# Kernel tuning notes

Measured on AMD Instinct MI355X. Metric: run time of the kernel, lower is better.

The kernel has to match this reference:

```python
import jax, jax.numpy as jnp
import numpy as np

B, S, D, H, HID = 4, 1024, 1024, 16, 4096
DK = D // H
EPS = 1e-6


def _ln(x):
    # LayerNorm without affine, eps=1e-6
    mu = jnp.mean(x, axis=-1, keepdims=True)
    var = jnp.var(x, axis=-1, keepdims=True)
    return (x - mu) / jnp.sqrt(var + EPS)


def _lin(x, W, b):
    # torch Linear convention: W is [out, in]
    y = jnp.einsum('...i,oi->...o', x, W)
    return y + b if b is not None else y


def setup_inputs() -> dict:
    key = jax.random.key(0)
    ks = jax.random.split(key, 16)
    sc = lambda fan_in: 1.0 / np.sqrt(fan_in)
    inp = {
        'x': jax.random.normal(ks[0], (B, S, D), jnp.float32),
        'cond': jax.random.normal(ks[1], (B, 1, D), jnp.float32),
        'Wq': jax.random.normal(ks[2], (D, D), jnp.float32) * sc(D),
        'bq': jnp.zeros((D,), jnp.float32),
        'Wk': jax.random.normal(ks[3], (D, D), jnp.float32) * sc(D),
        'bk': jnp.zeros((D,), jnp.float32),
        'Wv': jax.random.normal(ks[4], (D, D), jnp.float32) * sc(D),
        'bv': jnp.zeros((D,), jnp.float32),
        'Wo': jax.random.normal(ks[5], (D, D), jnp.float32) * sc(D),
        'bo': jnp.zeros((D,), jnp.float32),
        'W1': jax.random.normal(ks[6], (HID, D), jnp.float32) * sc(D),
        'b1': jnp.zeros((HID,), jnp.float32),
        'W2': jax.random.normal(ks[7], (D, HID), jnp.float32) * sc(HID),
        'b2': jnp.zeros((D,), jnp.float32),
        'Wada': jax.random.normal(ks[8], (6 * D, D), jnp.float32) * sc(D),
        'bada': jnp.zeros((6 * D,), jnp.float32),
    }
    return inp


def reference(x, cond, Wq, bq, Wk, bk, Wv, bv, Wo, bo, W1, b1, W2, b2, Wada, bada):
    # adaLN modulation: SiLU -> Linear -> chunk 6 along last dim
    mod = _lin(jax.nn.silu(cond), Wada, bada)  # [B,1,6D]
    gama1, beta1, alpha1, gama2, beta2, alpha2 = jnp.split(mod, 6, axis=-1)

    # attention branch
    residual = x
    h = _ln(x) * (1.0 + beta1) + gama1  # modulate(shift=gama1, scale=beta1)
    q = _lin(h, Wq, bq).reshape(B, S, H, DK)
    k = _lin(h, Wk, bk).reshape(B, S, H, DK)
    v = _lin(h, Wv, bv).reshape(B, S, H, DK)
    scores = jnp.einsum('bqhd,bkhd->bhqk', q, k) / jnp.sqrt(jnp.float32(DK))
    probs = jax.nn.softmax(scores, axis=-1)
    attn = jnp.einsum('bhqk,bkhd->bqhd', probs, v).reshape(B, S, D)
    attn = _lin(attn, Wo, bo)
    x = residual + alpha1 * attn

    # MLP branch
    residual = x
    h = _ln(x) * (1.0 + beta2) + gama2
    h = _lin(h, W1, b1)
    h = jax.nn.gelu(h, approximate=False)  # torch nn.GELU default (erf)
    h = _lin(h, W2, b2)
    return residual + alpha2 * h
```

## Files before the change

### kernel.cpp

```cpp
#include <hip/hip_runtime.h>
#include <cstdint>

typedef __bf16 bf16_t;
typedef __bf16 bf16x4 __attribute__((ext_vector_type(4)));
typedef __bf16 bf16x8 __attribute__((ext_vector_type(8)));
typedef float f32x4 __attribute__((ext_vector_type(4)));

#define B_ 4
#define S_ 1024
#define D_ 1024
#define HID_ 4096
#define MEG (1u << 20)

static const size_t OFF_WBF  = 0;
static const size_t OFF_BQKV = 25165824;
static const size_t OFF_MOD  = 25178112;
static const size_t OFF_H    = 25276416;
static const size_t OFF_QKV  = 33665024;
static const size_t OFF_VT   = 58830848;
static const size_t OFF_ATTN = 67219456;
static const size_t OFF_X1   = 75608064;
static const size_t OFF_PART = 92385280;
static const size_t OFF_MLPH = 159494144;

__device__ __forceinline__ void async_copy16(const bf16_t* g, bf16_t* l) {
  __builtin_amdgcn_global_load_lds(
      (__attribute__((address_space(1))) void*)(g),
      (__attribute__((address_space(3))) void*)(l), 16, 0, 0);
}

__global__ __launch_bounds__(256) void convert_pack(
    const float* __restrict__ Wq, const float* __restrict__ Wk,
    const float* __restrict__ Wv, const float* __restrict__ Wo,
    const float* __restrict__ W1, const float* __restrict__ W2,
    const float* __restrict__ bq, const float* __restrict__ bk,
    const float* __restrict__ bv, bf16_t* __restrict__ wbf,
    float* __restrict__ bqkv) {
  const int y = blockIdx.y;
  if (y == 6) {
    int i = blockIdx.x * 256 + threadIdx.x;
    if (i < 3072)
      bqkv[i] = i < 1024 ? bq[i] : (i < 2048 ? bk[i - 1024] : bv[i - 2048]);
    return;
  }
  const float* src; bf16_t* dst; int n;
  switch (y) {
    case 0: src = Wq; dst = wbf;           n = MEG;     break;
    case 1: src = Wk; dst = wbf + MEG;     n = MEG;     break;
    case 2: src = Wv; dst = wbf + 2*MEG;   n = MEG;     break;
    case 3: src = Wo; dst = wbf + 3*MEG;   n = MEG;     break;
    case 4: src = W1; dst = wbf + 4*MEG;   n = 4*MEG;   break;
    default: src = W2; dst = wbf + 8*MEG;  n = 4*MEG;   break;
  }
  int idx = (blockIdx.x * 256 + threadIdx.x) * 4;
  if (idx < n) {
    float4 v = *(const float4*)(src + idx);
    bf16x4 pk;
    pk.x = (__bf16)v.x; pk.y = (__bf16)v.y; pk.z = (__bf16)v.z; pk.w = (__bf16)v.w;
    *(bf16x4*)(dst + idx) = pk;
  }
}

__global__ __launch_bounds__(256) void ada_mod(
    const float* __restrict__ cond, const float* __restrict__ Wada,
    const float* __restrict__ bada, float* __restrict__ mod) {
  const int wave = threadIdx.x >> 6, lane = threadIdx.x & 63;
  const int gw = blockIdx.x * 4 + wave;
  const int b = gw / 6144, o = gw % 6144;
  const float* cb = cond + b * D_;
  const float* wr = Wada + (size_t)o * D_;
  float acc = 0.f;
#pragma unroll
  for (int l = 0; l < 16; l++) {
    int i = l * 64 + lane;
    float c = cb[i];
    float s = c / (1.0f + __expf(-c));
    acc += s * wr[i];
  }
#pragma unroll
  for (int offs = 32; offs; offs >>= 1) acc += __shfl_xor(acc, offs);
  if (lane == 0) mod[gw] = acc + bada[o];
}

__global__ __launch_bounds__(256) void ln_modulate(
    const float* __restrict__ X, const float* __restrict__ mod,
    bf16_t* __restrict__ H, int goff) {
  const int row = blockIdx.x;
  const int b = row >> 10;
  const int t = threadIdx.x;
  const float* xr = X + (size_t)row * D_;
  float4 xv = *(const float4*)(xr + t * 4);
  float s = xv.x + xv.y + xv.z + xv.w;
  float q = xv.x*xv.x + xv.y*xv.y + xv.z*xv.z + xv.w*xv.w;
  const int wave = t >> 6, lane = t & 63;
#pragma unroll
  for (int offs = 32; offs; offs >>= 1) {
    s += __shfl_down(s, offs);
    q += __shfl_down(q, offs);
  }
  __shared__ float sb[4][2];
  if (lane == 0) { sb[wave][0] = s; sb[wave][1] = q; }
  __syncthreads();
  float st = sb[0][0] + sb[1][0] + sb[2][0] + sb[3][0];
  float qt = sb[0][1] + sb[1][1] + sb[2][1] + sb[3][1];
  float mu = st * (1.0f / D_);
  float var = qt * (1.0f / D_) - mu * mu;
  float rstd = rsqrtf(var + 1e-6f);
  const float* mb = mod + (size_t)b * 6144 + goff;
  const int c = t * 4;
  float4 gm = *(const float4*)(mb + c);
  float4 bt = *(const float4*)(mb + 1024 + c);
  bf16x4 pk;
  pk.x = (__bf16)((xv.x - mu) * rstd * (1.0f + bt.x) + gm.x);
  pk.y = (__bf16)((xv.y - mu) * rstd * (1.0f + bt.y) + gm.y);
  pk.z = (__bf16)((xv.z - mu) * rstd * (1.0f + bt.z) + gm.z);
  pk.w = (__bf16)((xv.w - mu) * rstd * (1.0f + bt.w) + gm.w);
  *(bf16x4*)(H + (size_t)row * D_ + c) = pk;
}

__global__ __launch_bounds__(256) void transpose_v(
    const bf16_t* __restrict__ qkv, bf16_t* __restrict__ vT) {
  __shared__ bf16_t tile[64][65];
  const int bh = blockIdx.y;
  const int b = bh >> 4, hh = bh & 15;
  const int s0 = blockIdx.x * 64;
  const int t = threadIdx.x;
  const int tx = t & 63, ty = t >> 6;
  const bf16_t* src = qkv + (size_t)b * S_ * 3072 + 2048 + hh * 64;
  for (int r = ty; r < 64; r += 4)
    tile[r][tx] = src[(size_t)(s0 + r) * 3072 + tx];
  __syncthreads();
  bf16_t* dst = vT + (size_t)bh * 64 * 1024;
  for (int r = ty; r < 64; r += 4)
    dst[(size_t)r * 1024 + s0 + tx] = tile[tx][r];
}

__global__ __launch_bounds__(256) void flash_attn(
    const bf16_t* __restrict__ qkv, const bf16_t* __restrict__ vT,
    bf16_t* __restrict__ attn) {
  __shared__ __align__(16) bf16_t Qs[64 * 64];
  __shared__ __align__(16) bf16_t Ks[128 * 64];
  __shared__ __align__(16) bf16_t Vs[64 * 128];
  __shared__ __align__(16) bf16_t Ps[4 * 16 * 136];

  const int t = threadIdx.x;
  const int wave = t >> 6, lane = t & 63;
  const int lm = lane & 15, quad = lane >> 4;
  const int bh = blockIdx.y;
  const int b = bh >> 4, hh = bh & 15;
  const int s0 = blockIdx.x * 64;

  const bf16_t* qbase = qkv + (size_t)b * S_ * 3072 + hh * 64;
  const bf16_t* kbase = qbase + 1024;
  const bf16_t* vbase = vT + (size_t)bh * (64 * 1024);

#pragma unroll
  for (int j = 0; j < 2; j++) {
    int slot = j * 256 + t;
    int row = slot >> 3;
    int cg = (slot & 7) ^ (row & 7);
    async_copy16(qbase + (size_t)(s0 + row) * 3072 + cg * 8, &Qs[slot * 8]);
  }

  f32x4 accO[4] = {};
  float mrow[4], lrow[4];
#pragma unroll
  for (int r = 0; r < 4; r++) { mrow[r] = -1e30f; lrow[r] = 0.f; }

  bf16_t* Pw = &Ps[wave * 16 * 136];

  for (int k0 = 0; k0 < S_; k0 += 128) {
    __syncthreads();
#pragma unroll
    for (int j = 0; j < 4; j++) {
      int slot = j * 256 + t;
      int row = slot >> 3;
      int cg = (slot & 7) ^ (row & 7);
      async_copy16(kbase + (size_t)(k0 + row) * 3072 + cg * 8, &Ks[slot * 8]);
    }
#pragma unroll
    for (int j = 0; j < 4; j++) {
      int slot = j * 256 + t;
      int row = slot >> 4;
      int cp = slot & 15;
      int cg = (cp & 8) | ((cp & 7) ^ (row & 7));
      async_copy16(vbase + (size_t)row * 1024 + k0 + cg * 8, &Vs[slot * 8]);
    }
    __syncthreads();

    f32x4 accS[8] = {};
#pragma unroll
    for (int ks = 0; ks < 2; ks++) {
      int rq = wave * 16 + lm;
      int cq = (ks * 4 + quad) ^ (rq & 7);
      bf16x8 aq = *(const bf16x8*)&Qs[rq * 64 + cq * 8];
#pragma unroll
      for (int ni = 0; ni < 8; ni++) {
        int rk = ni * 16 + lm;
        int ck = (ks * 4 + quad) ^ (rk & 7);
        bf16x8 bk8 = *(const bf16x8*)&Ks[rk * 64 + ck * 8];
        accS[ni] = __builtin_amdgcn_mfma_f32_16x16x32_bf16(aq, bk8, accS[ni], 0, 0, 0);
      }
    }

    float alpha[4];
#pragma unroll
    for (int r = 0; r < 4; r++) {
      float mx = accS[0][r];
#pragma unroll
      for (int ni = 1; ni < 8; ni++) mx = fmaxf(mx, accS[ni][r]);
      mx = fmaxf(mx, __shfl_xor(mx, 1));
      mx = fmaxf(mx, __shfl_xor(mx, 2));
      mx = fmaxf(mx, __shfl_xor(mx, 4));
      mx = fmaxf(mx, __shfl_xor(mx, 8));
      mx *= 0.125f;
      float mnew = fmaxf(mrow[r], mx);
      alpha[r] = __expf(mrow[r] - mnew);
      mrow[r] = mnew;
      float sum = 0.f;
#pragma unroll
      for (int ni = 0; ni < 8; ni++) {
        float p = __expf(accS[ni][r] * 0.125f - mnew);
        accS[ni][r] = p;
        sum += p;
      }
      sum += __shfl_xor(sum, 1);
      sum += __shfl_xor(sum, 2);
      sum += __shfl_xor(sum, 4);
      sum += __shfl_xor(sum, 8);
      lrow[r] = lrow[r] * alpha[r] + sum;
    }
#pragma unroll
    for (int di = 0; di < 4; di++)
#pragma unroll
      for (int r = 0; r < 4; r++) accO[di][r] *= alpha[r];

#pragma unroll
    for (int ni = 0; ni < 8; ni++)
#pragma unroll
      for (int r = 0; r < 4; r++)
        Pw[(quad * 4 + r) * 136 + ni * 16 + lm] = (__bf16)accS[ni][r];

#pragma unroll
    for (int ks2 = 0; ks2 < 4; ks2++) {
      bf16x8 ap = *(const bf16x8*)&Pw[lm * 136 + ks2 * 32 + quad * 8];
#pragma unroll
      for (int di = 0; di < 4; di++) {
        int rv = di * 16 + lm;
        int g = ks2 * 4 + quad;
        int cp = (g & 8) | ((g & 7) ^ (rv & 7));
        bf16x8 bv = *(const bf16x8*)&Vs[rv * 128 + cp * 8];
        accO[di] = __builtin_amdgcn_mfma_f32_16x16x32_bf16(ap, bv, accO[di], 0, 0, 0);
      }
    }
  }

#pragma unroll
  for (int r = 0; r < 4; r++) {
    float inv = 1.0f / lrow[r];
    int row = quad * 4 + r;
#pragma unroll
    for (int di = 0; di < 4; di++) {
      int col = di * 16 + lm;
      int cph = (col >> 3) ^ (row & 7);
      Pw[row * 64 + cph * 8 + (col & 7)] = (__bf16)(accO[di][r] * inv);
    }
  }
  bf16_t* abase = attn + (size_t)b * S_ * 1024 +
                  (size_t)(s0 + wave * 16) * 1024 + hh * 64;
#pragma unroll
  for (int it = 0; it < 2; it++) {
    int slot = it * 64 + lane;
    int row = slot >> 3;
    int cg = slot & 7;
    int cph = cg ^ (row & 7);
    bf16x8 val = *(const bf16x8*)&Pw[row * 64 + cph * 8];
    *(bf16x8*)(abase + (size_t)row * 1024 + cg * 8) = val;
  }
}

template <int EPI>
__global__ __launch_bounds__(256) void gemm_bt(
    const bf16_t* __restrict__ A, int lda, long long sAz,
    const bf16_t* __restrict__ B, int ldb, long long sBz,
    void* __restrict__ Cv, int ldc, long long sCz,
    int M, int N, int K,
    const float* __restrict__ bias,
    float scale) {
  __shared__ __align__(16) bf16_t As[2][128 * 32];
  __shared__ __align__(16) bf16_t Bs[2][128 * 32];

  const int z = blockIdx.z;
  A += (size_t)z * sAz;
  B += (size_t)z * sBz;

  const int t = threadIdx.x;
  const int wave = t >> 6;
  const int lane = t & 63;
  const int lm = lane & 15;
  const int quad = lane >> 4;
  const int wr = wave >> 1;
  const int wc = wave & 1;

  const int m0 = blockIdx.y * 128;
  const int n0 = blockIdx.x * 128;

  f32x4 acc[4][4] = {};

  const int srow = t >> 2;
  const int gch = (t & 3) ^ (srow & 3);
  const int lds_off = t * 8;
  const bf16_t* Ap0 = A + (size_t)(m0 + srow) * lda + gch * 8;
  const bf16_t* Ap1 = A + (size_t)(m0 + 64 + srow) * lda + gch * 8;
  const bf16_t* Bp0 = B + (size_t)(n0 + srow) * ldb + gch * 8;
  const bf16_t* Bp1 = B + (size_t)(n0 + 64 + srow) * ldb + gch * 8;

  const int niter = K >> 5;
  async_copy16(Ap0, &As[0][lds_off]);
  async_copy16(Ap1, &As[0][2048 + lds_off]);
  async_copy16(Bp0, &Bs[0][lds_off]);
  async_copy16(Bp1, &Bs[0][2048 + lds_off]);

  for (int it = 0; it < niter; ++it) {
    asm volatile("s_waitcnt vmcnt(0)\n\ts_barrier" ::: "memory");
    if (it + 1 < niter) {
      const int ko = (it + 1) << 5;
      const int nb = (it + 1) & 1;
      async_copy16(Ap0 + ko, &As[nb][lds_off]);
      async_copy16(Ap1 + ko, &As[nb][2048 + lds_off]);
      async_copy16(Bp0 + ko, &Bs[nb][lds_off]);
      async_copy16(Bp1 + ko, &Bs[nb][2048 + lds_off]);
    }
    const int cb = it & 1;
    bf16x8 af[4], bfr[4];
#pragma unroll
    for (int i = 0; i < 4; i++) {
      int ra = wr * 64 + i * 16 + lm;
      af[i] = *(const bf16x8*)&As[cb][ra * 32 + ((quad ^ (ra & 3)) * 8)];
      int rb = wc * 64 + i * 16 + lm;
      bfr[i] = *(const bf16x8*)&Bs[cb][rb * 32 + ((quad ^ (rb & 3)) * 8)];
    }
#pragma unroll
    for (int mi = 0; mi < 4; mi++)
#pragma unroll
      for (int ni = 0; ni < 4; ni++)
        acc[mi][ni] = __builtin_amdgcn_mfma_f32_16x16x32_bf16(
            af[mi], bfr[ni], acc[mi][ni], 0, 0, 0);
  }

  const size_t cz = (size_t)z * sCz;
#pragma unroll
  for (int mi = 0; mi < 4; mi++) {
#pragma unroll
    for (int ni = 0; ni < 4; ni++) {
#pragma unroll
      for (int r = 0; r < 4; r++) {
        int row = m0 + wr * 64 + mi * 16 + quad * 4 + r;
        int col = n0 + wc * 64 + ni * 16 + lm;
        float v = acc[mi][ni][r];
        size_t idx = cz + (size_t)row * ldc + col;
        if (EPI == 1) {
          ((float*)Cv)[idx] = v * scale;
        } else if (EPI == 0) {
          if (bias) v += bias[col];
          ((bf16_t*)Cv)[idx] = (__bf16)v;
        } else if (EPI == 3) {
          v += bias[col];
          float u = 1.5957691216f * (v + 0.044715f * v * v * v);
          float g = v / (1.0f + __expf(-u));
          ((bf16_t*)Cv)[idx] = (__bf16)g;
        }
      }
    }
  }
}

__global__ __launch_bounds__(256) void reduce_ln(
    const float* __restrict__ part, const float* __restrict__ x,
    const float* __restrict__ bo, const float* __restrict__ mod,
    float* __restrict__ x1, bf16_t* __restrict__ h) {
  const int row = blockIdx.x;
  const int b = row >> 10;
  const int t = threadIdx.x;
  const int c = t * 4;
  const size_t idx = (size_t)row * 1024 + c;
  float4 p0 = *(const float4*)(part + idx);
  float4 p1 = *(const float4*)(part + 4194304 + idx);
  float4 bb = *(const float4*)(bo + c);
  float4 al = *(const float4*)(mod + (size_t)b * 6144 + 2048 + c);
  float4 xs = *(const float4*)(x + idx);
  float4 xv;
  xv.x = xs.x + al.x * (p0.x + p1.x + bb.x);
  xv.y = xs.y + al.y * (p0.y + p1.y + bb.y);
  xv.z = xs.z + al.z * (p0.z + p1.z + bb.z);
  xv.w = xs.w + al.w * (p0.w + p1.w + bb.w);
  *(float4*)(x1 + idx) = xv;

  float s = xv.x + xv.y + xv.z + xv.w;
  float q = xv.x*xv.x + xv.y*xv.y + xv.z*xv.z + xv.w*xv.w;
  const int wave = t >> 6, lane = t & 63;
#pragma unroll
  for (int offs = 32; offs; offs >>= 1) {
    s += __shfl_down(s, offs);
    q += __shfl_down(q, offs);
  }
  __shared__ float sb[4][2];
  if (lane == 0) { sb[wave][0] = s; sb[wave][1] = q; }
  __syncthreads();
  float st = sb[0][0] + sb[1][0] + sb[2][0] + sb[3][0];
  float qt = sb[0][1] + sb[1][1] + sb[2][1] + sb[3][1];
  float mu = st * (1.0f / D_);
  float var = qt * (1.0f / D_) - mu * mu;
  float rstd = rsqrtf(var + 1e-6f);
  const float* mb = mod + (size_t)b * 6144 + 3072;
  float4 gm = *(const float4*)(mb + c);
  float4 bt = *(const float4*)(mb + 1024 + c);
  bf16x4 pk;
  pk.x = (__bf16)((xv.x - mu) * rstd * (1.0f + bt.x) + gm.x);
  pk.y = (__bf16)((xv.y - mu) * rstd * (1.0f + bt.y) + gm.y);
  pk.z = (__bf16)((xv.z - mu) * rstd * (1.0f + bt.z) + gm.z);
  pk.w = (__bf16)((xv.w - mu) * rstd * (1.0f + bt.w) + gm.w);
  *(bf16x4*)(h + idx) = pk;
}

__global__ __launch_bounds__(256) void reduce_w2(
    const float* __restrict__ part, const float* __restrict__ x1,
    const float* __restrict__ b2, const float* __restrict__ mod,
    float* __restrict__ out) {
  const int idx = (blockIdx.x * 256 + threadIdx.x) * 4;
  const int col = idx & 1023;
  const int row = idx >> 10;
  const int b = row >> 10;
  float4 s0 = *(const float4*)(part + idx);
  float4 s1 = *(const float4*)(part + 4194304 + idx);
  float4 s2 = *(const float4*)(part + 8388608 + idx);
  float4 s3 = *(const float4*)(part + 12582912 + idx);
  float4 bb = *(const float4*)(b2 + col);
  float4 al = *(const float4*)(mod + (size_t)b * 6144 + 5120 + col);
  float4 rs = *(const float4*)(x1 + idx);
  float4 o;
  o.x = rs.x + al.x * (s0.x + s1.x + s2.x + s3.x + bb.x);
  o.y = rs.y + al.y * (s0.y + s1.y + s2.y + s3.y + bb.y);
  o.z = rs.z + al.z * (s0.z + s1.z + s2.z + s3.z + bb.z);
  o.w = rs.w + al.w * (s0.w + s1.w + s2.w + s3.w + bb.w);
  *(float4*)(out + idx) = o;
}

extern "C" void kernel_launch(void* const* d_in, const int* in_sizes, int n_in,
                              void* d_out, int out_size, void* d_ws, size_t ws_size,
                              hipStream_t stream) {
  (void)in_sizes; (void)n_in; (void)out_size; (void)ws_size;
  const float* x    = (const float*)d_in[0];
  const float* cond = (const float*)d_in[1];
  const float* Wq   = (const float*)d_in[2];
  const float* bq   = (const float*)d_in[3];
  const float* Wk   = (const float*)d_in[4];
  const float* bk   = (const float*)d_in[5];
  const float* Wv   = (const float*)d_in[6];
  const float* bv   = (const float*)d_in[7];
  const float* Wo   = (const float*)d_in[8];
  const float* bo   = (const float*)d_in[9];
  const float* W1   = (const float*)d_in[10];
  const float* b1   = (const float*)d_in[11];
  const float* W2   = (const float*)d_in[12];
  const float* b2   = (const float*)d_in[13];
  const float* Wada = (const float*)d_in[14];
  const float* bada = (const float*)d_in[15];

  uint8_t* ws = (uint8_t*)d_ws;
  bf16_t* wbf   = (bf16_t*)(ws + OFF_WBF);
  float*  bqkv  = (float*)(ws + OFF_BQKV);
  float*  mod   = (float*)(ws + OFF_MOD);
  bf16_t* h     = (bf16_t*)(ws + OFF_H);
  bf16_t* qkv   = (bf16_t*)(ws + OFF_QKV);
  bf16_t* vT    = (bf16_t*)(ws + OFF_VT);
  bf16_t* attn  = (bf16_t*)(ws + OFF_ATTN);
  float*  x1    = (float*)(ws + OFF_X1);
  float*  part  = (float*)(ws + OFF_PART);
  bf16_t* mlph  = (bf16_t*)(ws + OFF_MLPH);
  float* out = (float*)d_out;

  convert_pack<<<dim3(4096, 7, 1), 256, 0, stream>>>(Wq, Wk, Wv, Wo, W1, W2,
                                                     bq, bk, bv, wbf, bqkv);
  ada_mod<<<6144, 256, 0, stream>>>(cond, Wada, bada, mod);
  ln_modulate<<<4096, 256, 0, stream>>>(x, mod, h, 0);
  gemm_bt<0><<<dim3(24, 32, 1), 256, 0, stream>>>(
      h, 1024, 0, wbf, 1024, 0, qkv, 3072, 0, 4096, 3072, 1024,
      bqkv, 1.f);
  transpose_v<<<dim3(16, 64, 1), 256, 0, stream>>>(qkv, vT);
  flash_attn<<<dim3(16, 64, 1), 256, 0, stream>>>(qkv, vT, attn);

  gemm_bt<1><<<dim3(8, 32, 2), 256, 0, stream>>>(
      attn, 1024, 512, wbf + (size_t)3 * MEG, 1024, 512, part, 1024, 4194304,
      4096, 1024, 512, nullptr, 1.f);
  reduce_ln<<<4096, 256, 0, stream>>>(part, x, bo, mod, x1, h);

  gemm_bt<3><<<dim3(32, 32, 1), 256, 0, stream>>>(
      h, 1024, 0, wbf + (size_t)4 * MEG, 1024, 0, mlph, 4096, 0,
      4096, 4096, 1024, b1, 1.f);
  gemm_bt<1><<<dim3(8, 32, 4), 256, 0, stream>>>(
      mlph, 4096, 1024, wbf + (size_t)8 * MEG, 4096, 1024, part, 1024, 4194304,
      4096, 1024, 1024, nullptr, 1.f);
  reduce_w2<<<4096, 256, 0, stream>>>(part, x1, b2, mod, out);
}
```

Baseline: 429.1 us.

## Remap GEMM tiles per XCD, retune LDS swizzle, halve W2 split-K, batch adaLN

The GEMM block index is remapped so each XCD works on a contiguous band of row tiles and nearby column panels, aiming for better L2 reuse. The LDS XOR swizzle now keys on (row>>1) instead of row, to cut bank conflicts in the fragment reads. The W2 GEMM drops from 4-way to 2-way split-K, which halves the fp32 partial traffic written and read by reduce_w2, at the cost of a longer K loop per block and half as many blocks. adaLN now computes all 4 batches per Wada row, so each weight row is read once instead of four times. The tile remap hardcodes 8 XCDs and a grid height of 32.

```diff
diff --git a/kernel.cpp b/kernel.cpp
--- a/kernel.cpp
+++ b/kernel.cpp
@@ -65,21 +65,33 @@
     const float* __restrict__ cond, const float* __restrict__ Wada,
     const float* __restrict__ bada, float* __restrict__ mod) {
   const int wave = threadIdx.x >> 6, lane = threadIdx.x & 63;
-  const int gw = blockIdx.x * 4 + wave;
-  const int b = gw / 6144, o = gw % 6144;
-  const float* cb = cond + b * D_;
+  const int o = blockIdx.x * 4 + wave;
   const float* wr = Wada + (size_t)o * D_;
-  float acc = 0.f;
+  float a0 = 0.f, a1 = 0.f, a2 = 0.f, a3 = 0.f;
 #pragma unroll
   for (int l = 0; l < 16; l++) {
     int i = l * 64 + lane;
-    float c = cb[i];
-    float s = c / (1.0f + __expf(-c));
-    acc += s * wr[i];
-  }
-#pragma unroll
-  for (int offs = 32; offs; offs >>= 1) acc += __shfl_xor(acc, offs);
-  if (lane == 0) mod[gw] = acc + bada[o];
+    float w = wr[i];
+    float c0 = cond[i], c1 = cond[1024 + i], c2 = cond[2048 + i], c3 = cond[3072 + i];
+    a0 += w * (c0 / (1.0f + __expf(-c0)));
+    a1 += w * (c1 / (1.0f + __expf(-c1)));
+    a2 += w * (c2 / (1.0f + __expf(-c2)));
+    a3 += w * (c3 / (1.0f + __expf(-c3)));
+  }
+#pragma unroll
+  for (int offs = 32; offs; offs >>= 1) {
+    a0 += __shfl_xor(a0, offs);
+    a1 += __shfl_xor(a1, offs);
+    a2 += __shfl_xor(a2, offs);
+    a3 += __shfl_xor(a3, offs);
+  }
+  if (lane == 0) {
+    float bb = bada[o];
+    mod[o]          = a0 + bb;
+    mod[6144 + o]   = a1 + bb;
+    mod[12288 + o]  = a2 + bb;
+    mod[18432 + o]  = a3 + bb;
+  }
 }
 
 __global__ __launch_bounds__(256) void ln_modulate(
@@ -294,81 +306,88 @@
   A += (size_t)z * sAz;
   B += (size_t)z * sBz;
 
-  const int t = threadIdx.x;
-  const int wave = t >> 6;
-  const int lane = t & 63;
-  const int lm = lane & 15;
-  const int quad = lane >> 4;
-  const int wr = wave >> 1;
-  const int wc = wave & 1;
-
-  const int m0 = blockIdx.y * 128;
-  const int n0 = blockIdx.x * 128;
-
-  f32x4 acc[4][4] = {};
-
-  const int srow = t >> 2;
-  const int gch = (t & 3) ^ (srow & 3);
-  const int lds_off = t * 8;
-  const bf16_t* Ap0 = A + (size_t)(m0 + srow) * lda + gch * 8;
-  const bf16_t* Ap1 = A + (size_t)(m0 + 64 + srow) * lda + gch * 8;
-  const bf16_t* Bp0 = B + (size_t)(n0 + srow) * ldb + gch * 8;
-  const bf16_t* Bp1 = B + (size_t)(n0 + 64 + srow) * ldb + gch * 8;
-
-  const int niter = K >> 5;
-  async_copy16(Ap0, &As[0][lds_off]);
-  async_copy16(Ap1, &As[0][2048 + lds_off]);
-  async_copy16(Bp0, &Bs[0][lds_off]);
-  async_copy16(Bp1, &Bs[0][2048 + lds_off]);
-
-  for (int it = 0; it < niter; ++it) {
-    asm volatile("s_waitcnt vmcnt(0)\n\ts_barrier" ::: "memory");
-    if (it + 1 < niter) {
-      const int ko = (it + 1) << 5;
-      const int nb = (it + 1) & 1;
-      async_copy16(Ap0 + ko, &As[nb][lds_off]);
-      async_copy16(Ap1 + ko, &As[nb][2048 + lds_off]);
-      async_copy16(Bp0 + ko, &Bs[nb][lds_off]);
-      async_copy16(Bp1 + ko, &Bs[nb][2048 + lds_off]);
-    }
-    const int cb = it & 1;
-    bf16x8 af[4], bfr[4];
-#pragma unroll
-    for (int i = 0; i < 4; i++) {
-      int ra = wr * 64 + i * 16 + lm;
-      af[i] = *(const bf16x8*)&As[cb][ra * 32 + ((quad ^ (ra & 3)) * 8)];
-      int rb = wc * 64 + i * 16 + lm;
-      bfr[i] = *(const bf16x8*)&Bs[cb][rb * 32 + ((quad ^ (rb & 3)) * 8)];
-    }
-#pragma unroll
-    for (int mi = 0; mi < 4; mi++)
-#pragma unroll
-      for (int ni = 0; ni < 4; ni++)
-        acc[mi][ni] = __builtin_amdgcn_mfma_f32_16x16x32_bf16(
-            af[mi], bfr[ni], acc[mi][ni], 0, 0, 0);
-  }
-
-  const size_t cz = (size_t)z * sCz;
-#pragma unroll
-  for (int mi = 0; mi < 4; mi++) {
-#pragma unroll
-    for (int ni = 0; ni < 4; ni++) {
-#pragma unroll
-      for (int r = 0; r < 4; r++) {
-        int row = m0 + wr * 64 + mi * 16 + quad * 4 + r;
-        int col = n0 + wc * 64 + ni * 16 + lm;
-        float v = acc[mi][ni][r];
-        size_t idx = cz + (size_t)row * ldc + col;
-        if (EPI == 1) {
-          ((float*)Cv)[idx] = v * scale;
-        } else if (EPI == 0) {
-          if (bias) v += bias[col];
-          ((bf16_t*)Cv)[idx] = (__bf16)v;
-        } else if (EPI == 3) {
-          v += bias[col];
-          float u = 1.5957691216f * (v + 0.044715f * v * v * v);
-          float g = v / (1.0f + __expf(-u));
-          ((bf16_t*)Cv)[idx] = (__bf16)g;
+  {
+    int d = blockIdx.x + gridDim.x * blockIdx.y;
+    int xcd = d & 7, sId = d >> 3;
+    int qq = sId & 31, panel = sId >> 5;
+    const int bx = panel * 8 + (qq >> 2);
+    const int by = xcd * 4 + (qq & 3);
+    const int t = threadIdx.x;
+    const int wave = t >> 6;
+    const int lane = t & 63;
+    const int lm = lane & 15;
+    const int quad = lane >> 4;
+    const int wr = wave >> 1;
+    const int wc = wave & 1;
+
+    const int m0 = by * 128;
+    const int n0 = bx * 128;
+
+    f32x4 acc[4][4] = {};
+
+    const int srow = t >> 2;
+    const int gch = (t & 3) ^ ((srow >> 1) & 3);
+    const int lds_off = t * 8;
+    const bf16_t* Ap0 = A + (size_t)(m0 + srow) * lda + gch * 8;
+    const bf16_t* Ap1 = A + (size_t)(m0 + 64 + srow) * lda + gch * 8;
+    const bf16_t* Bp0 = B + (size_t)(n0 + srow) * ldb + gch * 8;
+    const bf16_t* Bp1 = B + (size_t)(n0 + 64 + srow) * ldb + gch * 8;
+
+    const int sOff = (quad ^ ((lm >> 1) & 3)) * 8;
+
+    const int niter = K >> 5;
+    async_copy16(Ap0, &As[0][lds_off]);
+    async_copy16(Ap1, &As[0][2048 + lds_off]);
+    async_copy16(Bp0, &Bs[0][lds_off]);
+    async_copy16(Bp1, &Bs[0][2048 + lds_off]);
+
+    for (int it = 0; it < niter; ++it) {
+      asm volatile("s_waitcnt vmcnt(0)\n\ts_barrier" ::: "memory");
+      if (it + 1 < niter) {
+        const int ko = (it + 1) << 5;
+        const int nb = (it + 1) & 1;
+        async_copy16(Ap0 + ko, &As[nb][lds_off]);
+        async_copy16(Ap1 + ko, &As[nb][2048 + lds_off]);
+        async_copy16(Bp0 + ko, &Bs[nb][lds_off]);
+        async_copy16(Bp1 + ko, &Bs[nb][2048 + lds_off]);
+      }
+      const int cb = it & 1;
+      bf16x8 af[4], bfr[4];
+#pragma unroll
+      for (int i = 0; i < 4; i++) {
+        af[i] = *(const bf16x8*)&As[cb][(wr * 64 + i * 16 + lm) * 32 + sOff];
+        bfr[i] = *(const bf16x8*)&Bs[cb][(wc * 64 + i * 16 + lm) * 32 + sOff];
+      }
+#pragma unroll
+      for (int mi = 0; mi < 4; mi++)
+#pragma unroll
+        for (int ni = 0; ni < 4; ni++)
+          acc[mi][ni] = __builtin_amdgcn_mfma_f32_16x16x32_bf16(
+              af[mi], bfr[ni], acc[mi][ni], 0, 0, 0);
+    }
+
+    const size_t cz = (size_t)z * sCz;
+#pragma unroll
+    for (int mi = 0; mi < 4; mi++) {
+#pragma unroll
+      for (int ni = 0; ni < 4; ni++) {
+#pragma unroll
+        for (int r = 0; r < 4; r++) {
+          int row = m0 + wr * 64 + mi * 16 + quad * 4 + r;
+          int col = n0 + wc * 64 + ni * 16 + lm;
+          float v = acc[mi][ni][r];
+          size_t idx = cz + (size_t)row * ldc + col;
+          if (EPI == 1) {
+            ((float*)Cv)[idx] = v * scale;
+          } else if (EPI == 0) {
+            if (bias) v += bias[col];
+            ((bf16_t*)Cv)[idx] = (__bf16)v;
+          } else if (EPI == 3) {
+            v += bias[col];
+            float u = 1.5957691216f * (v + 0.044715f * v * v * v);
+            float g = v / (1.0f + __expf(-u));
+            ((bf16_t*)Cv)[idx] = (__bf16)g;
+          }
         }
       }
     }
@@ -433,16 +452,14 @@
   const int b = row >> 10;
   float4 s0 = *(const float4*)(part + idx);
   float4 s1 = *(const float4*)(part + 4194304 + idx);
-  float4 s2 = *(const float4*)(part + 8388608 + idx);
-  float4 s3 = *(const float4*)(part + 12582912 + idx);
   float4 bb = *(const float4*)(b2 + col);
   float4 al = *(const float4*)(mod + (size_t)b * 6144 + 5120 + col);
   float4 rs = *(const float4*)(x1 + idx);
   float4 o;
-  o.x = rs.x + al.x * (s0.x + s1.x + s2.x + s3.x + bb.x);
-  o.y = rs.y + al.y * (s0.y + s1.y + s2.y + s3.y + bb.y);
-  o.z = rs.z + al.z * (s0.z + s1.z + s2.z + s3.z + bb.z);
-  o.w = rs.w + al.w * (s0.w + s1.w + s2.w + s3.w + bb.w);
+  o.x = rs.x + al.x * (s0.x + s1.x + bb.x);
+  o.y = rs.y + al.y * (s0.y + s1.y + bb.y);
+  o.z = rs.z + al.z * (s0.z + s1.z + bb.z);
+  o.w = rs.w + al.w * (s0.w + s1.w + bb.w);
   *(float4*)(out + idx) = o;
 }
 
@@ -482,7 +499,7 @@
 
   convert_pack<<<dim3(4096, 7, 1), 256, 0, stream>>>(Wq, Wk, Wv, Wo, W1, W2,
                                                      bq, bk, bv, wbf, bqkv);
-  ada_mod<<<6144, 256, 0, stream>>>(cond, Wada, bada, mod);
+  ada_mod<<<1536, 256, 0, stream>>>(cond, Wada, bada, mod);
   ln_modulate<<<4096, 256, 0, stream>>>(x, mod, h, 0);
   gemm_bt<0><<<dim3(24, 32, 1), 256, 0, stream>>>(
       h, 1024, 0, wbf, 1024, 0, qkv, 3072, 0, 4096, 3072, 1024,
@@ -498,8 +515,8 @@
   gemm_bt<3><<<dim3(32, 32, 1), 256, 0, stream>>>(
       h, 1024, 0, wbf + (size_t)4 * MEG, 1024, 0, mlph, 4096, 0,
       4096, 4096, 1024, b1, 1.f);
-  gemm_bt<1><<<dim3(8, 32, 4), 256, 0, stream>>>(
-      mlph, 4096, 1024, wbf + (size_t)8 * MEG, 4096, 1024, part, 1024, 4194304,
-      4096, 1024, 1024, nullptr, 1.f);
+  gemm_bt<1><<<dim3(8, 32, 2), 256, 0, stream>>>(
+      mlph, 4096, 2048, wbf + (size_t)8 * MEG, 4096, 2048, part, 1024, 4194304,
+      4096, 1024, 2048, nullptr, 1.f);
   reduce_w2<<<4096, 256, 0, stream>>>(part, x1, b2, mod, out);
 }
```

Result: faster. 401.2 us (-6.5%).
